# Performance work log

Hardware: AMD Instinct MI355X
Metric: run time of the kernel (lower is better)

The kernel has to match this reference:

```python
import jax, jax.numpy as jnp
import numpy as np

N_NODES = 100000


def gcn_conv(x, W, b, src, dst, norm, n_nodes):
    # x: [N, F_in] -> [N, F_out]; GCNConv: D^-1/2 (A+I) D^-1/2 (X W) + b
    h = x @ W                                   # [N, F_out]
    msg = h[src] * norm[:, None]                # [E+N, F_out] gather + scale
    out = jax.ops.segment_sum(msg, dst, num_segments=n_nodes)  # scatter-add
    return out + b


def setup_inputs() -> dict:
    key = jax.random.key(0)
    k0, k1, k2, k3, k4, k5 = jax.random.split(key, 6)
    n, e, f_in, f_hid, n_cls = N_NODES, 1600000, 128, 128, 3
    x = jax.random.normal(k0, (n, f_in), dtype=jnp.float32)
    edge_index = jax.random.randint(k1, (2, e), 0, n, dtype=jnp.int64)
    s1 = 1.0 / np.sqrt(f_in)
    s2 = 1.0 / np.sqrt(f_hid)
    W1 = jax.random.uniform(k2, (f_in, f_hid), jnp.float32, -s1, s1)
    b1 = jnp.zeros((f_hid,), jnp.float32)
    W2 = jax.random.uniform(k3, (f_hid, f_hid), jnp.float32, -s2, s2)
    b2 = jnp.zeros((f_hid,), jnp.float32)
    Wfc = jax.random.uniform(k4, (f_hid, n_cls), jnp.float32, -s2, s2)
    bfc = jax.random.uniform(k5, (n_cls,), jnp.float32, -s2, s2)
    return {"x": x, "edge_index": edge_index, "W1": W1, "b1": b1,
            "W2": W2, "b2": b2, "Wfc": Wfc, "bfc": bfc}


def reference(x, edge_index, W1, b1, W2, b2, Wfc, bfc):
    n = x.shape[0]
    # add self-loops (PyG GCNConv default add_self_loops=True)
    loops = jnp.arange(n, dtype=edge_index.dtype)
    src = jnp.concatenate([edge_index[0], loops])
    dst = jnp.concatenate([edge_index[1], loops])
    deg = jax.ops.segment_sum(jnp.ones_like(dst, dtype=x.dtype), dst,
                              num_segments=n)
    dinv = jax.lax.rsqrt(deg)                   # deg >= 1 due to self-loops
    norm = dinv[src] * dinv[dst]                # [E+N]
    h = jax.nn.relu(gcn_conv(x, W1, b1, src, dst, norm, n))   # dropout=eval id
    h = jax.nn.relu(gcn_conv(h, W2, b2, src, dst, norm, n))
    return jnp.tanh(h @ Wfc + bfc)              # [N, 3]
```

## Files before the change

### kernel.cpp

```cpp
#include <hip/hip_runtime.h>
#include <hip/hip_bf16.h>
#include <hip/hip_fp16.h>


#define NODE_F 128

typedef __attribute__((ext_vector_type(8))) short bf16x8;
typedef __attribute__((ext_vector_type(8))) unsigned short u16x8;
typedef __attribute__((ext_vector_type(4))) float f32x4;

__device__ inline unsigned short bf16_rn(float x) {
    unsigned u = __builtin_bit_cast(unsigned, x);
    unsigned r = (u + 0x7fffu + ((u >> 16) & 1u)) >> 16;
    return (unsigned short)r;
}
__device__ inline float bf16_to_f(unsigned short h) {
    unsigned u = (unsigned)h << 16;
    return __builtin_bit_cast(float, u);
}


__global__ __launch_bounds__(256) void wconv_kernel(const float* __restrict__ W1,
                                                    const float* __restrict__ W2,
                                                    unsigned short* __restrict__ WhiT,
                                                    unsigned short* __restrict__ WloT)
{
    const float* W = blockIdx.x ? W2 : W1;
    unsigned short* hiT = WhiT + blockIdx.x * 128 * 128;
    unsigned short* loT = WloT + blockIdx.x * 128 * 128;
    int tid = threadIdx.x;
    for (int i = tid; i < 128 * 128; i += 256) {
        int k = i >> 7, n = i & 127;
        float x = W[i];
        unsigned short hi = bf16_rn(x);
        float lo = x - bf16_to_f(hi);
        hiT[n * 128 + k] = hi;
        loT[n * 128 + k] = bf16_rn(lo);
    }
}


__global__ __launch_bounds__(256) void scan_block_kernel(
    const int* __restrict__ degE, int* __restrict__ row_start,
    int* __restrict__ bsum, int N)
{
    __shared__ int s[256];
    const int tid = threadIdx.x;
    const int idx = blockIdx.x * 1024 + tid * 4;
    int v0 = (idx + 0 < N) ? degE[idx + 0] : 0;
    int v1 = (idx + 1 < N) ? degE[idx + 1] : 0;
    int v2 = (idx + 2 < N) ? degE[idx + 2] : 0;
    int v3 = (idx + 3 < N) ? degE[idx + 3] : 0;
    int t = v0 + v1 + v2 + v3;
    s[tid] = t;
    __syncthreads();
    #pragma unroll
    for (int off = 1; off < 256; off <<= 1) {
        int x = (tid >= off) ? s[tid - off] : 0;
        __syncthreads();
        s[tid] += x;
        __syncthreads();
    }
    int excl = s[tid] - t;
    if (idx + 0 < N) row_start[idx + 0] = excl;
    if (idx + 1 < N) row_start[idx + 1] = excl + v0;
    if (idx + 2 < N) row_start[idx + 2] = excl + v0 + v1;
    if (idx + 3 < N) row_start[idx + 3] = excl + v0 + v1 + v2;
    if (tid == 255) bsum[blockIdx.x] = s[255];
}

__global__ __launch_bounds__(1024) void scan_tops_kernel(int* __restrict__ bsum, int nb) {
    __shared__ int s[1024];
    const int tid = threadIdx.x;
    int v = (tid < nb) ? bsum[tid] : 0;
    s[tid] = v;
    __syncthreads();
    #pragma unroll
    for (int off = 1; off < 1024; off <<= 1) {
        int x = (tid >= off) ? s[tid - off] : 0;
        __syncthreads();
        s[tid] += x;
        __syncthreads();
    }
    if (tid < nb) bsum[tid] = s[tid] - v;
}

__global__ void scan_finish_kernel(const int* __restrict__ degE, int* __restrict__ row_start,
                                   const int* __restrict__ bsum, float* __restrict__ dinv, int N)
{
    int i = blockIdx.x * blockDim.x + threadIdx.x;
    if (i >= N) return;
    int rs = row_start[i] + bsum[i >> 10];
    row_start[i] = rs;
    dinv[i] = rsqrtf((float)degE[i] + 1.0f);
    if (i == N - 1) row_start[N] = rs + degE[i];
}


template<bool SPLIT_IN, bool SCALE_OUT>
__device__ __forceinline__ void gemm_body(
    const float* __restrict__ Xf,
    const unsigned short* __restrict__ Xhi_g, const unsigned short* __restrict__ Xlo_g,
    const unsigned short* __restrict__ WhiT, const unsigned short* __restrict__ WloT,
    const float* __restrict__ dinv,
    __half* __restrict__ Hout, int N, int bid,
    unsigned short* xhi, unsigned short* xlo)
{
    const int tid  = threadIdx.x;
    const int lane = tid & 63;
    const int w    = tid >> 6;
    const int rbase = bid * 64;

    bf16x8 bhi[2][4], blo[2][4];
    {
        int n0   = w * 32 + (lane & 15);
        int koct = (lane >> 4) * 8;
        #pragma unroll
        for (int nt = 0; nt < 2; ++nt) {
            #pragma unroll
            for (int kk = 0; kk < 4; ++kk) {
                size_t o = (size_t)(n0 + nt * 16) * 128 + kk * 32 + koct;
                bhi[nt][kk] = *reinterpret_cast<const bf16x8*>(WhiT + o);
                blo[nt][kk] = *reinterpret_cast<const bf16x8*>(WloT + o);
            }
        }
    }

    if (!SPLIT_IN) {
        #pragma unroll
        for (int it = 0; it < 8; ++it) {
            int f   = it * 256 + tid;
            int row = f >> 5;
            int k4  = f & 31;
            float4 v = make_float4(0.f, 0.f, 0.f, 0.f);
            if (rbase + row < N)
                v = *reinterpret_cast<const float4*>(Xf + (size_t)(rbase + row) * NODE_F + k4 * 4);
            float xs[4] = {v.x, v.y, v.z, v.w};
            ushort4 h4, l4;
            unsigned short* hp = &h4.x;
            unsigned short* lp = &l4.x;
            #pragma unroll
            for (int j = 0; j < 4; ++j) {
                unsigned short hi = bf16_rn(xs[j]);
                hp[j] = hi;
                lp[j] = bf16_rn(xs[j] - bf16_to_f(hi));
            }
            int byte = row * 256 + ((k4 * 8) ^ ((row & 7) << 4));
            *reinterpret_cast<ushort4*>(reinterpret_cast<char*>(xhi) + byte) = h4;
            *reinterpret_cast<ushort4*>(reinterpret_cast<char*>(xlo) + byte) = l4;
        }
    } else {
        #pragma unroll
        for (int it = 0; it < 4; ++it) {
            int idx = it * 256 + tid;
            int row = idx >> 4;
            int k8  = idx & 15;
            u16x8 h = {0, 0, 0, 0, 0, 0, 0, 0};
            u16x8 l = {0, 0, 0, 0, 0, 0, 0, 0};
            if (rbase + row < N) {
                size_t g = (size_t)(rbase + row) * NODE_F + k8 * 8;
                h = *reinterpret_cast<const u16x8*>(Xhi_g + g);
                l = *reinterpret_cast<const u16x8*>(Xlo_g + g);
            }
            int byte = row * 256 + ((k8 * 16) ^ ((row & 7) << 4));
            *reinterpret_cast<u16x8*>(reinterpret_cast<char*>(xhi) + byte) = h;
            *reinterpret_cast<u16x8*>(reinterpret_cast<char*>(xlo) + byte) = l;
        }
    }
    __syncthreads();

    f32x4 acc[4][2];
    #pragma unroll
    for (int m = 0; m < 4; ++m)
        #pragma unroll
        for (int nt = 0; nt < 2; ++nt)
            acc[m][nt] = (f32x4){0.f, 0.f, 0.f, 0.f};

    #pragma unroll
    for (int kk = 0; kk < 4; ++kk) {
        #pragma unroll
        for (int m = 0; m < 4; ++m) {
            int row  = m * 16 + (lane & 15);
            int koff = kk * 64 + (lane >> 4) * 16;
            int byte = row * 256 + (koff ^ ((row & 7) << 4));
            bf16x8 ahi = *reinterpret_cast<const bf16x8*>(reinterpret_cast<char*>(xhi) + byte);
            bf16x8 alo = *reinterpret_cast<const bf16x8*>(reinterpret_cast<char*>(xlo) + byte);
            #pragma unroll
            for (int nt = 0; nt < 2; ++nt) {
                acc[m][nt] = __builtin_amdgcn_mfma_f32_16x16x32_bf16(ahi, bhi[nt][kk], acc[m][nt], 0, 0, 0);
                acc[m][nt] = __builtin_amdgcn_mfma_f32_16x16x32_bf16(ahi, blo[nt][kk], acc[m][nt], 0, 0, 0);
                acc[m][nt] = __builtin_amdgcn_mfma_f32_16x16x32_bf16(alo, bhi[nt][kk], acc[m][nt], 0, 0, 0);
            }
        }
    }

    #pragma unroll
    for (int m = 0; m < 4; ++m) {
        int row = rbase + m * 16 + (lane >> 4) * 4;
        int col = w * 32 + (lane & 15);
        #pragma unroll
        for (int nt = 0; nt < 2; ++nt) {
            #pragma unroll
            for (int r = 0; r < 4; ++r) {
                if (row + r < N) {
                    float v = acc[m][nt][r];
                    if (SCALE_OUT) v *= dinv[row + r];
                    Hout[(size_t)(row + r) * NODE_F + col + nt * 16] = __float2half(v);
                }
            }
        }
    }
}


__global__ __launch_bounds__(256) void hybridA_kernel(
    const int* __restrict__ dst, int* __restrict__ degE, int* __restrict__ rank,
    int E, int deg_blocks,
    const float* __restrict__ X, const unsigned short* __restrict__ WhiT,
    const unsigned short* __restrict__ WloT, __half* __restrict__ H, int N)
{
    __shared__ unsigned short xhi[64 * 128];
    __shared__ unsigned short xlo[64 * 128];
    if ((int)blockIdx.x < deg_blocks) {
        int e = blockIdx.x * 256 + threadIdx.x;
        if (e < E) rank[e] = atomicAdd(&degE[dst[e]], 1);
    } else {
        gemm_body<false, false>(X, nullptr, nullptr, WhiT, WloT, nullptr,
                                H, N, blockIdx.x - deg_blocks, xhi, xlo);
    }
}


__global__ __launch_bounds__(256) void hybridB_kernel(
    const int* __restrict__ src, const int* __restrict__ dst,
    const int* __restrict__ rank, const int* __restrict__ row_start,
    int* __restrict__ csr_src, int E, int fill_blocks,
    __half* __restrict__ H, const int* __restrict__ degE, int N)
{
    if ((int)blockIdx.x < fill_blocks) {
        int e = blockIdx.x * 256 + threadIdx.x;
        if (e < E) csr_src[row_start[dst[e]] + rank[e]] = src[e];
    } else {
        int idx = (blockIdx.x - fill_blocks) * 256 + threadIdx.x;
        if (idx < N * 16) {
            int row = idx >> 4;
            float ds = rsqrtf((float)degE[row] + 1.0f);
            __half2* p = reinterpret_cast<__half2*>(H) + (size_t)idx * 4;
            #pragma unroll
            for (int j = 0; j < 4; ++j) {
                float2 v = __half22float2(p[j]);
                v.x *= ds; v.y *= ds;
                p[j] = __float22half2_rn(v);
            }
        }
    }
}


__global__ __launch_bounds__(256) void gather1_kernel(
    const __half* __restrict__ Hs, const int* __restrict__ csr_src,
    const int* __restrict__ row_start, const float* __restrict__ dinv,
    const float* __restrict__ b,
    unsigned short* __restrict__ Xhi, unsigned short* __restrict__ Xlo, int N)
{
    int node = (blockIdx.x * blockDim.x + threadIdx.x) >> 6;
    int lane = threadIdx.x & 63;
    if (node >= N) return;

    const __half2* H2 = reinterpret_cast<const __half2*>(Hs);
    float2 a = __half22float2(H2[(size_t)node * 64 + lane]);

    int i   = row_start[node];
    int end = row_start[node + 1];
    for (; i + 7 < end; i += 8) {
        int s0 = csr_src[i + 0], s1 = csr_src[i + 1], s2 = csr_src[i + 2], s3 = csr_src[i + 3];
        int s4 = csr_src[i + 4], s5 = csr_src[i + 5], s6 = csr_src[i + 6], s7 = csr_src[i + 7];
        float2 v0 = __half22float2(H2[(size_t)s0 * 64 + lane]);
        float2 v1 = __half22float2(H2[(size_t)s1 * 64 + lane]);
        float2 v2 = __half22float2(H2[(size_t)s2 * 64 + lane]);
        float2 v3 = __half22float2(H2[(size_t)s3 * 64 + lane]);
        float2 v4 = __half22float2(H2[(size_t)s4 * 64 + lane]);
        float2 v5 = __half22float2(H2[(size_t)s5 * 64 + lane]);
        float2 v6 = __half22float2(H2[(size_t)s6 * 64 + lane]);
        float2 v7 = __half22float2(H2[(size_t)s7 * 64 + lane]);
        a.x += ((v0.x + v1.x) + (v2.x + v3.x)) + ((v4.x + v5.x) + (v6.x + v7.x));
        a.y += ((v0.y + v1.y) + (v2.y + v3.y)) + ((v4.y + v5.y) + (v6.y + v7.y));
    }
    for (; i < end; ++i) {
        int s = csr_src[i];
        float2 v = __half22float2(H2[(size_t)s * 64 + lane]);
        a.x += v.x;
        a.y += v.y;
    }

    const float dd = dinv[node];
    float2 bb = reinterpret_cast<const float2*>(b)[lane];
    float rx = fmaxf(bb.x + dd * a.x, 0.f);
    float ry = fmaxf(bb.y + dd * a.y, 0.f);
    unsigned short hx = bf16_rn(rx), hy = bf16_rn(ry);
    unsigned short lx = bf16_rn(rx - bf16_to_f(hx));
    unsigned short ly = bf16_rn(ry - bf16_to_f(hy));
    reinterpret_cast<ushort2*>(Xhi)[(size_t)node * 64 + lane] = make_ushort2(hx, hy);
    reinterpret_cast<ushort2*>(Xlo)[(size_t)node * 64 + lane] = make_ushort2(lx, ly);
}


__global__ __launch_bounds__(256) void gather2fc_kernel(
    const __half* __restrict__ Hs, const int* __restrict__ csr_src,
    const int* __restrict__ row_start, const float* __restrict__ dinv,
    const float* __restrict__ b, const float* __restrict__ Wfc,
    const float* __restrict__ bfc, float* __restrict__ out, int N)
{
    int node = (blockIdx.x * blockDim.x + threadIdx.x) >> 6;
    int lane = threadIdx.x & 63;
    if (node >= N) return;

    const __half2* H2 = reinterpret_cast<const __half2*>(Hs);
    float2 a = __half22float2(H2[(size_t)node * 64 + lane]);

    int i   = row_start[node];
    int end = row_start[node + 1];
    for (; i + 7 < end; i += 8) {
        int s0 = csr_src[i + 0], s1 = csr_src[i + 1], s2 = csr_src[i + 2], s3 = csr_src[i + 3];
        int s4 = csr_src[i + 4], s5 = csr_src[i + 5], s6 = csr_src[i + 6], s7 = csr_src[i + 7];
        float2 v0 = __half22float2(H2[(size_t)s0 * 64 + lane]);
        float2 v1 = __half22float2(H2[(size_t)s1 * 64 + lane]);
        float2 v2 = __half22float2(H2[(size_t)s2 * 64 + lane]);
        float2 v3 = __half22float2(H2[(size_t)s3 * 64 + lane]);
        float2 v4 = __half22float2(H2[(size_t)s4 * 64 + lane]);
        float2 v5 = __half22float2(H2[(size_t)s5 * 64 + lane]);
        float2 v6 = __half22float2(H2[(size_t)s6 * 64 + lane]);
        float2 v7 = __half22float2(H2[(size_t)s7 * 64 + lane]);
        a.x += ((v0.x + v1.x) + (v2.x + v3.x)) + ((v4.x + v5.x) + (v6.x + v7.x));
        a.y += ((v0.y + v1.y) + (v2.y + v3.y)) + ((v4.y + v5.y) + (v6.y + v7.y));
    }
    for (; i < end; ++i) {
        int s = csr_src[i];
        float2 v = __half22float2(H2[(size_t)s * 64 + lane]);
        a.x += v.x;
        a.y += v.y;
    }

    const float dd = dinv[node];
    float2 bb = reinterpret_cast<const float2*>(b)[lane];
    float rx = fmaxf(bb.x + dd * a.x, 0.f);
    float ry = fmaxf(bb.y + dd * a.y, 0.f);

    const float* w0 = Wfc + (size_t)(2 * lane) * 3;
    float p0 = rx * w0[0] + ry * w0[3];
    float p1 = rx * w0[1] + ry * w0[4];
    float p2 = rx * w0[2] + ry * w0[5];
    #pragma unroll
    for (int off = 32; off > 0; off >>= 1) {
        p0 += __shfl_down(p0, off);
        p1 += __shfl_down(p1, off);
        p2 += __shfl_down(p2, off);
    }
    if (lane == 0) {
        out[(size_t)node * 3 + 0] = tanhf(p0 + bfc[0]);
        out[(size_t)node * 3 + 1] = tanhf(p1 + bfc[1]);
        out[(size_t)node * 3 + 2] = tanhf(p2 + bfc[2]);
    }
}


__global__ __launch_bounds__(256) void gemm2_kernel(
    const unsigned short* __restrict__ Xhi_g, const unsigned short* __restrict__ Xlo_g,
    const unsigned short* __restrict__ WhiT, const unsigned short* __restrict__ WloT,
    const float* __restrict__ dinv, __half* __restrict__ Hs, int N)
{
    __shared__ unsigned short xhi[64 * 128];
    __shared__ unsigned short xlo[64 * 128];
    gemm_body<true, true>(nullptr, Xhi_g, Xlo_g, WhiT, WloT, dinv,
                          Hs, N, blockIdx.x, xhi, xlo);
}

extern "C" void kernel_launch(void* const* d_in, const int* in_sizes, int n_in,
                              void* d_out, int out_size, void* d_ws, size_t ws_size,
                              hipStream_t stream)
{
    const float* x    = (const float*)d_in[0];
    const int*   edge = (const int*)d_in[1];
    const float* W1   = (const float*)d_in[2];
    const float* b1   = (const float*)d_in[3];
    const float* W2   = (const float*)d_in[4];
    const float* b2   = (const float*)d_in[5];
    const float* Wfc  = (const float*)d_in[6];
    const float* bfc  = (const float*)d_in[7];
    float* out = (float*)d_out;

    const int N = in_sizes[0] / NODE_F;
    const int E = in_sizes[1] / 2;
    const int* src = edge;
    const int* dst = edge + E;

    char* ws = (char*)d_ws;
    size_t off = 0;
    auto alloc = [&](size_t bytes) {
        void* p = ws + off;
        off += (bytes + 511) & ~511ull;
        return p;
    };
    const int nblk1024 = (N + 1023) / 1024;
    float* dinv      = (float*)alloc((size_t)N * 4);
    int*   degE      = (int*)  alloc((size_t)N * 4);
    int*   rank      = (int*)  alloc((size_t)E * 4);
    int*   row_start = (int*)  alloc((size_t)(N + 1) * 4);
    int*   bsum      = (int*)  alloc((size_t)nblk1024 * 4);
    int*   csr_src   = (int*)  alloc((size_t)E * 4);
    unsigned short* WhiT = (unsigned short*)alloc(2 * 128 * 128 * 2);
    unsigned short* WloT = (unsigned short*)alloc(2 * 128 * 128 * 2);
    __half* Hs       = (__half*)alloc((size_t)N * NODE_F * 2);
    unsigned short* Xhi = (unsigned short*)alloc((size_t)N * NODE_F * 2);
    unsigned short* Xlo = (unsigned short*)alloc((size_t)N * NODE_F * 2);
    (void)ws_size; (void)n_in; (void)out_size;

    const int B = 256;
    const int gemm_grid   = (N + 63) / 64;
    const int edge_grid   = (E + B - 1) / B;
    const int scale_grid  = (N * 16 + B - 1) / B;
    const int gather_grid = (N + 3) / 4;

    wconv_kernel<<<2, B, 0, stream>>>(W1, W2, WhiT, WloT);
    hipMemsetAsync(degE, 0, (size_t)N * 4, stream);

    hybridA_kernel<<<edge_grid + gemm_grid, B, 0, stream>>>(
        dst, degE, rank, E, edge_grid, x, WhiT, WloT, Hs, N);

    scan_block_kernel<<<nblk1024, B, 0, stream>>>(degE, row_start, bsum, N);
    scan_tops_kernel<<<1, 1024, 0, stream>>>(bsum, nblk1024);
    scan_finish_kernel<<<(N + B - 1) / B, B, 0, stream>>>(degE, row_start, bsum, dinv, N);

    hybridB_kernel<<<edge_grid + scale_grid, B, 0, stream>>>(
        src, dst, rank, row_start, csr_src, E, edge_grid, Hs, degE, N);

    gather1_kernel<<<gather_grid, B, 0, stream>>>(Hs, csr_src, row_start, dinv, b1, Xhi, Xlo, N);

    gemm2_kernel<<<gemm_grid, B, 0, stream>>>(Xhi, Xlo, WhiT + 128 * 128, WloT + 128 * 128,
                                              dinv, Hs, N);

    gather2fc_kernel<<<gather_grid, B, 0, stream>>>(Hs, csr_src, row_start, dinv, b2,
                                                    Wfc, bfc, out, N);
}
```

Measured before the change: 352.0 us.

## Split gather wave into two half-waves with 8-byte loads; fold degree count into GEMM blocks

The gather kernels now have each wave's two 32-lane halves process alternating neighbours. Each lane loads 4 fp16 values as one 8-byte load, and the halves are combined with a cross-half shuffle. This doubles bytes per load instruction and halves the serial neighbour loop length per lane. Separately, the hybrid kernel that split blocks between degree counting and GEMM is replaced by one where every GEMM block first runs a grid-stride loop of degree atomics and then does its GEMM tile. This may delay the GEMM work and unbalance blocks.

```diff
diff --git a/kernel.cpp b/kernel.cpp
--- a/kernel.cpp
+++ b/kernel.cpp
@@ -17,6 +17,12 @@
 __device__ inline float bf16_to_f(unsigned short h) {
     unsigned u = (unsigned)h << 16;
     return __builtin_bit_cast(float, u);
+}
+__device__ inline void acc4_h(float a[4], uint2 v) {
+    __half2 h01 = __builtin_bit_cast(__half2, v.x);
+    __half2 h23 = __builtin_bit_cast(__half2, v.y);
+    float2 f01 = __half22float2(h01), f23 = __half22float2(h23);
+    a[0] += f01.x; a[1] += f01.y; a[2] += f23.x; a[3] += f23.y;
 }
 
 
@@ -213,21 +219,18 @@
 }
 
 
-__global__ __launch_bounds__(256) void hybridA_kernel(
-    const int* __restrict__ dst, int* __restrict__ degE, int* __restrict__ rank,
-    int E, int deg_blocks,
+__global__ __launch_bounds__(256) void gemm1deg_kernel(
+    const int* __restrict__ dst, int* __restrict__ degE, int* __restrict__ rank, int E,
+    int total_threads,
     const float* __restrict__ X, const unsigned short* __restrict__ WhiT,
     const unsigned short* __restrict__ WloT, __half* __restrict__ H, int N)
 {
     __shared__ unsigned short xhi[64 * 128];
     __shared__ unsigned short xlo[64 * 128];
-    if ((int)blockIdx.x < deg_blocks) {
-        int e = blockIdx.x * 256 + threadIdx.x;
-        if (e < E) rank[e] = atomicAdd(&degE[dst[e]], 1);
-    } else {
-        gemm_body<false, false>(X, nullptr, nullptr, WhiT, WloT, nullptr,
-                                H, N, blockIdx.x - deg_blocks, xhi, xlo);
-    }
+    for (int e = blockIdx.x * 256 + threadIdx.x; e < E; e += total_threads)
+        rank[e] = atomicAdd(&degE[dst[e]], 1);
+    gemm_body<false, false>(X, nullptr, nullptr, WhiT, WloT, nullptr,
+                            H, N, blockIdx.x, xhi, xlo);
 }
 
 
@@ -257,6 +260,42 @@
 }
 
 
+__device__ __forceinline__ void gather_core(
+    const __half* __restrict__ Hs, const int* __restrict__ csr_src,
+    const int* __restrict__ row_start, int node, int li, int h, float a[4])
+{
+    const char* Hb = reinterpret_cast<const char*>(Hs);
+    a[0] = a[1] = a[2] = a[3] = 0.f;
+    if (h == 0)
+        acc4_h(a, *reinterpret_cast<const uint2*>(Hb + ((size_t)node * 256 + li * 8)));
+
+    int i   = row_start[node];
+    int end = row_start[node + 1];
+    for (; i + 7 < end; i += 8) {
+        int s0 = csr_src[i + 0 + h];
+        int s1 = csr_src[i + 2 + h];
+        int s2 = csr_src[i + 4 + h];
+        int s3 = csr_src[i + 6 + h];
+        uint2 v0 = *reinterpret_cast<const uint2*>(Hb + ((size_t)s0 * 256 + li * 8));
+        uint2 v1 = *reinterpret_cast<const uint2*>(Hb + ((size_t)s1 * 256 + li * 8));
+        uint2 v2 = *reinterpret_cast<const uint2*>(Hb + ((size_t)s2 * 256 + li * 8));
+        uint2 v3 = *reinterpret_cast<const uint2*>(Hb + ((size_t)s3 * 256 + li * 8));
+        acc4_h(a, v0); acc4_h(a, v1); acc4_h(a, v2); acc4_h(a, v3);
+    }
+    for (; i + 1 < end; i += 2) {
+        int s = csr_src[i + h];
+        acc4_h(a, *reinterpret_cast<const uint2*>(Hb + ((size_t)s * 256 + li * 8)));
+    }
+    if (i < end && h == 0) {
+        int s = csr_src[i];
+        acc4_h(a, *reinterpret_cast<const uint2*>(Hb + ((size_t)s * 256 + li * 8)));
+    }
+    #pragma unroll
+    for (int j = 0; j < 4; ++j)
+        a[j] += __shfl_xor(a[j], 32);
+}
+
+
 __global__ __launch_bounds__(256) void gather1_kernel(
     const __half* __restrict__ Hs, const int* __restrict__ csr_src,
     const int* __restrict__ row_start, const float* __restrict__ dinv,
@@ -265,43 +304,27 @@
 {
     int node = (blockIdx.x * blockDim.x + threadIdx.x) >> 6;
     int lane = threadIdx.x & 63;
+    int li = lane & 31, h = lane >> 5;
     if (node >= N) return;
 
-    const __half2* H2 = reinterpret_cast<const __half2*>(Hs);
-    float2 a = __half22float2(H2[(size_t)node * 64 + lane]);
-
-    int i   = row_start[node];
-    int end = row_start[node + 1];
-    for (; i + 7 < end; i += 8) {
-        int s0 = csr_src[i + 0], s1 = csr_src[i + 1], s2 = csr_src[i + 2], s3 = csr_src[i + 3];
-        int s4 = csr_src[i + 4], s5 = csr_src[i + 5], s6 = csr_src[i + 6], s7 = csr_src[i + 7];
-        float2 v0 = __half22float2(H2[(size_t)s0 * 64 + lane]);
-        float2 v1 = __half22float2(H2[(size_t)s1 * 64 + lane]);
-        float2 v2 = __half22float2(H2[(size_t)s2 * 64 + lane]);
-        float2 v3 = __half22float2(H2[(size_t)s3 * 64 + lane]);
-        float2 v4 = __half22float2(H2[(size_t)s4 * 64 + lane]);
-        float2 v5 = __half22float2(H2[(size_t)s5 * 64 + lane]);
-        float2 v6 = __half22float2(H2[(size_t)s6 * 64 + lane]);
-        float2 v7 = __half22float2(H2[(size_t)s7 * 64 + lane]);
-        a.x += ((v0.x + v1.x) + (v2.x + v3.x)) + ((v4.x + v5.x) + (v6.x + v7.x));
-        a.y += ((v0.y + v1.y) + (v2.y + v3.y)) + ((v4.y + v5.y) + (v6.y + v7.y));
-    }
-    for (; i < end; ++i) {
-        int s = csr_src[i];
-        float2 v = __half22float2(H2[(size_t)s * 64 + lane]);
-        a.x += v.x;
-        a.y += v.y;
-    }
-
-    const float dd = dinv[node];
-    float2 bb = reinterpret_cast<const float2*>(b)[lane];
-    float rx = fmaxf(bb.x + dd * a.x, 0.f);
-    float ry = fmaxf(bb.y + dd * a.y, 0.f);
-    unsigned short hx = bf16_rn(rx), hy = bf16_rn(ry);
-    unsigned short lx = bf16_rn(rx - bf16_to_f(hx));
-    unsigned short ly = bf16_rn(ry - bf16_to_f(hy));
-    reinterpret_cast<ushort2*>(Xhi)[(size_t)node * 64 + lane] = make_ushort2(hx, hy);
-    reinterpret_cast<ushort2*>(Xlo)[(size_t)node * 64 + lane] = make_ushort2(lx, ly);
+    float a[4];
+    gather_core(Hs, csr_src, row_start, node, li, h, a);
+
+    if (h == 0) {
+        const float dd = dinv[node];
+        float4 bb = *reinterpret_cast<const float4*>(b + li * 4);
+        float r0 = fmaxf(bb.x + dd * a[0], 0.f);
+        float r1 = fmaxf(bb.y + dd * a[1], 0.f);
+        float r2 = fmaxf(bb.z + dd * a[2], 0.f);
+        float r3 = fmaxf(bb.w + dd * a[3], 0.f);
+        ushort4 h4, l4;
+        h4.x = bf16_rn(r0); l4.x = bf16_rn(r0 - bf16_to_f(h4.x));
+        h4.y = bf16_rn(r1); l4.y = bf16_rn(r1 - bf16_to_f(h4.y));
+        h4.z = bf16_rn(r2); l4.z = bf16_rn(r2 - bf16_to_f(h4.z));
+        h4.w = bf16_rn(r3); l4.w = bf16_rn(r3 - bf16_to_f(h4.w));
+        *reinterpret_cast<ushort4*>(Xhi + (size_t)node * NODE_F + li * 4) = h4;
+        *reinterpret_cast<ushort4*>(Xlo + (size_t)node * NODE_F + li * 4) = l4;
+    }
 }
 
 
@@ -313,45 +336,24 @@
 {
     int node = (blockIdx.x * blockDim.x + threadIdx.x) >> 6;
     int lane = threadIdx.x & 63;
+    int li = lane & 31, h = lane >> 5;
     if (node >= N) return;
 
-    const __half2* H2 = reinterpret_cast<const __half2*>(Hs);
-    float2 a = __half22float2(H2[(size_t)node * 64 + lane]);
-
-    int i   = row_start[node];
-    int end = row_start[node + 1];
-    for (; i + 7 < end; i += 8) {
-        int s0 = csr_src[i + 0], s1 = csr_src[i + 1], s2 = csr_src[i + 2], s3 = csr_src[i + 3];
-        int s4 = csr_src[i + 4], s5 = csr_src[i + 5], s6 = csr_src[i + 6], s7 = csr_src[i + 7];
-        float2 v0 = __half22float2(H2[(size_t)s0 * 64 + lane]);
-        float2 v1 = __half22float2(H2[(size_t)s1 * 64 + lane]);
-        float2 v2 = __half22float2(H2[(size_t)s2 * 64 + lane]);
-        float2 v3 = __half22float2(H2[(size_t)s3 * 64 + lane]);
-        float2 v4 = __half22float2(H2[(size_t)s4 * 64 + lane]);
-        float2 v5 = __half22float2(H2[(size_t)s5 * 64 + lane]);
-        float2 v6 = __half22float2(H2[(size_t)s6 * 64 + lane]);
-        float2 v7 = __half22float2(H2[(size_t)s7 * 64 + lane]);
-        a.x += ((v0.x + v1.x) + (v2.x + v3.x)) + ((v4.x + v5.x) + (v6.x + v7.x));
-        a.y += ((v0.y + v1.y) + (v2.y + v3.y)) + ((v4.y + v5.y) + (v6.y + v7.y));
-    }
-    for (; i < end; ++i) {
-        int s = csr_src[i];
-        float2 v = __half22float2(H2[(size_t)s * 64 + lane]);
-        a.x += v.x;
-        a.y += v.y;
-    }
+    float a[4];
+    gather_core(Hs, csr_src, row_start, node, li, h, a);
 
     const float dd = dinv[node];
-    float2 bb = reinterpret_cast<const float2*>(b)[lane];
-    float rx = fmaxf(bb.x + dd * a.x, 0.f);
-    float ry = fmaxf(bb.y + dd * a.y, 0.f);
-
-    const float* w0 = Wfc + (size_t)(2 * lane) * 3;
-    float p0 = rx * w0[0] + ry * w0[3];
-    float p1 = rx * w0[1] + ry * w0[4];
-    float p2 = rx * w0[2] + ry * w0[5];
-    #pragma unroll
-    for (int off = 32; off > 0; off >>= 1) {
+    float4 bb = *reinterpret_cast<const float4*>(b + li * 4);
+    float bv[4] = {bb.x, bb.y, bb.z, bb.w};
+    float p0 = 0.f, p1 = 0.f, p2 = 0.f;
+    #pragma unroll
+    for (int j = 0; j < 4; ++j) {
+        float r = fmaxf(bv[j] + dd * a[j], 0.f);
+        const float* wr = Wfc + (size_t)(li * 4 + j) * 3;
+        p0 += r * wr[0]; p1 += r * wr[1]; p2 += r * wr[2];
+    }
+    #pragma unroll
+    for (int off = 16; off > 0; off >>= 1) {
         p0 += __shfl_down(p0, off);
         p1 += __shfl_down(p1, off);
         p2 += __shfl_down(p2, off);
@@ -424,8 +426,8 @@
     wconv_kernel<<<2, B, 0, stream>>>(W1, W2, WhiT, WloT);
     hipMemsetAsync(degE, 0, (size_t)N * 4, stream);
 
-    hybridA_kernel<<<edge_grid + gemm_grid, B, 0, stream>>>(
-        dst, degE, rank, E, edge_grid, x, WhiT, WloT, Hs, N);
+    gemm1deg_kernel<<<gemm_grid, B, 0, stream>>>(
+        dst, degE, rank, E, gemm_grid * B, x, WhiT, WloT, Hs, N);
 
     scan_block_kernel<<<nblk1024, B, 0, stream>>>(degE, row_start, bsum, N);
     scan_tops_kernel<<<1, 1024, 0, stream>>>(bsum, nblk1024);
```

New measurement: 336.0 us. -4.5%, faster.
